# Kernel optimization log

Hardware: AMD Instinct MI355X
Metric: run time of the kernel (lower is better)

## Reference

```python
import jax, jax.numpy as jnp
import numpy as np

B, S, T = 32, 64, 64
D = 512          # model_size == controller hidden == cell_size
R = 4            # read heads
M = 64           # nr_cells
V = 10000        # vocab
IF = R * D + 3 * D + 5 * R + 3   # DNC interface vector size (3607)
NN_IN = D + R * D                # controller input: x + read vectors
CLIP = 20.0
EPS = 1e-6


def _cosine(mem, keys):
    # mem (B,m,w), keys (B,h,w) -> (B,h,m) batched cosine similarity
    mn = mem / (jnp.linalg.norm(mem, axis=2, keepdims=True) + EPS)
    kn = keys / (jnp.linalg.norm(keys, axis=2, keepdims=True) + EPS)
    return jnp.einsum('bhw,bmw->bhm', kn, mn)


def _allocate(usage):
    # usage (B,m) -> allocation weights (B,1,m)
    u = EPS + (1.0 - EPS) * usage
    phi = jnp.argsort(u, axis=1)                      # ascending: least used first
    su = jnp.take_along_axis(u, phi, axis=1)
    excl = jnp.cumprod(jnp.concatenate([jnp.ones_like(su[:, :1]), su[:, :-1]], axis=1), axis=1)
    sa = (1.0 - su) * excl
    return jnp.take_along_axis(sa, jnp.argsort(phi, axis=1), axis=1)[:, None, :]


def _memory_step(xi, st):
    memory, link, prec, rw, ww, usage = st
    b = xi.shape[0]
    # --- parse interface vector (same slicing as dnc.Memory, independent_linears=False) ---
    rk = jnp.tanh(xi[:, :R * D].reshape(b, R, D))                        # read keys
    rs = jax.nn.softplus(xi[:, R * D:R * D + R])                         # read strengths
    wk = jnp.tanh(xi[:, R * D + R:R * D + R + D].reshape(b, 1, D))       # write key
    ws = jax.nn.softplus(xi[:, R * D + R + D])[:, None]                  # write strength
    er = jax.nn.sigmoid(xi[:, R * D + R + D + 1:R * D + R + 2 * D + 1].reshape(b, 1, D))
    wv = jnp.tanh(xi[:, R * D + R + 2 * D + 1:R * D + R + 3 * D + 1].reshape(b, 1, D))
    fg = jax.nn.sigmoid(xi[:, R * D + R + 3 * D + 1:R * D + 2 * R + 3 * D + 1])   # free gates
    ag = jax.nn.sigmoid(xi[:, R * D + 2 * R + 3 * D + 1])[:, None, None]          # alloc gate
    wg = jax.nn.sigmoid(xi[:, R * D + 2 * R + 3 * D + 2])[:, None, None]          # write gate
    modes = jax.nn.softmax(xi[:, R * D + 2 * R + 3 * D + 3:R * D + 5 * R + 3 * D + 3].reshape(b, R, 3), axis=2)
    # --- write ---
    usage = usage + (1 - usage) * (1 - jnp.prod(1 - ww, axis=1))
    usage = usage * jnp.prod(1 - fg[:, :, None] * rw, axis=1)
    wcw = jax.nn.softmax(_cosine(memory, wk) * ws[:, :, None], axis=2)   # (B,1,M)
    alloc = _allocate(usage)
    ww = wg * (ag * alloc + (1 - ag) * wcw)                              # (B,1,M)
    reset = jnp.prod(1 - ww[:, :, :, None] * er[:, :, None, :], axis=1)  # (B,M,D)
    memory = memory * reset + jnp.einsum('bhm,bhw->bmw', ww, wv)
    ww_i, ww_j = ww[:, :, :, None], ww[:, :, None, :]
    link = (1 - ww_i - ww_j) * link + ww_i * prec[:, :, None, :]
    link = link * (1 - jnp.eye(M, dtype=link.dtype))                     # zero diagonal
    prec = (1 - jnp.sum(ww, axis=2, keepdims=True)) * prec + ww
    # --- read ---
    cw = jax.nn.softmax(_cosine(memory, rk) * rs[:, :, None], axis=2)    # (B,R,M)
    l0 = link[:, 0]
    fwd = jnp.einsum('bnm,brm->brn', l0, rw)
    bwd = jnp.einsum('bmn,brm->brn', l0, rw)
    rw = modes[:, :, 0:1] * bwd + modes[:, :, 1:2] * fwd + modes[:, :, 2:3] * cw
    rv = jnp.einsum('brm,bmw->brw', rw, memory)                          # read vectors
    return (memory, link, prec, rw, ww, usage), rv


def _lstm_cell(x, h, c, Wih, Whh, bih, bhh):
    g = x @ Wih.T + bih + h @ Whh.T + bhh
    i, f, gg, o = jnp.split(g, 4, axis=-1)
    c2 = jax.nn.sigmoid(f) * c + jax.nn.sigmoid(i) * jnp.tanh(gg)
    return jax.nn.sigmoid(o) * jnp.tanh(c2), c2


def _dnc_run(x, p, mem0):
    # x: (B,L,D). Faithful to ixaxaar dnc.py: each timestep input is concat(x_t, initial last_read=zeros).
    b, L, _ = x.shape
    xin = jnp.concatenate([x, jnp.zeros((b, L, R * D), x.dtype)], axis=-1)
    h = jnp.zeros((2, b, D), x.dtype)
    c = jnp.zeros((2, b, D), x.dtype)

    def step(carry, x_t):
        (h, c), mem = carry
        h0, c0 = _lstm_cell(x_t, h[0], c[0], p['Wih0'], p['Whh0'], p['bih0'], p['bhh0'])
        h1, c1 = _lstm_cell(h0, h[1], c[1], p['Wih1'], p['Whh1'], p['bih1'], p['bhh1'])
        out = jnp.clip(h1, -CLIP, CLIP)
        xi = out @ p['Wi'].T + p['bi']
        mem, rv = _memory_step(xi, mem)
        full = jnp.concatenate([out, rv.reshape(b, R * D)], axis=-1)
        y = full @ p['Wo'].T + p['bo']
        return ((jnp.stack([h0, h1]), jnp.stack([c0, c1])), mem), y

    (_, memT), ys = jax.lax.scan(step, ((h, c), mem0), jnp.swapaxes(xin, 0, 1))
    return jnp.swapaxes(ys, 0, 1), memT


def _init_mem(b, dtype):
    return (jnp.zeros((b, M, D), dtype), jnp.zeros((b, 1, M, M), dtype),
            jnp.zeros((b, 1, M), dtype), jnp.zeros((b, R, M), dtype),
            jnp.zeros((b, 1, M), dtype), jnp.zeros((b, M), dtype))


_PNAMES = ['Wih0', 'Whh0', 'bih0', 'bhh0', 'Wih1', 'Whh1', 'bih1', 'bhh1', 'Wi', 'bi', 'Wo', 'bo']


def setup_inputs() -> dict:
    key = jax.random.key(0)
    ks = iter(jax.random.split(key, 40))

    def p(shape, s=0.05):
        return jax.random.normal(next(ks), shape, dtype=jnp.float32) * s

    d = {'emb_src': p((V, D), 0.5), 'emb_tgt': p((V, D), 0.5)}
    shapes = [(4 * D, NN_IN), (4 * D, D), (4 * D,), (4 * D,), (4 * D, D), (4 * D, D), (4 * D,), (4 * D,),
              (IF, D), (IF,), (D, NN_IN), (D,)]
    for pre in ('enc', 'dec'):
        for n, sh in zip(_PNAMES, shapes):
            d[pre + '_' + n] = p(sh)
    d['fc_W'] = p((V, D))
    d['fc_b'] = p((V,))
    d['input'] = jax.random.randint(next(ks), (B, S), 0, V, dtype=jnp.int32)
    d['tgt'] = jax.random.randint(next(ks), (B, T), 0, V, dtype=jnp.int32)
    return d


def reference(emb_src, emb_tgt,
              enc_Wih0, enc_Whh0, enc_bih0, enc_bhh0, enc_Wih1, enc_Whh1, enc_bih1, enc_bhh1,
              enc_Wi, enc_bi, enc_Wo, enc_bo,
              dec_Wih0, dec_Whh0, dec_bih0, dec_bhh0, dec_Wih1, dec_Whh1, dec_bih1, dec_bhh1,
              dec_Wi, dec_bi, dec_Wo, dec_bo,
              fc_W, fc_b, input, tgt):
    enc_vals = [enc_Wih0, enc_Whh0, enc_bih0, enc_bhh0, enc_Wih1, enc_Whh1, enc_bih1, enc_bhh1,
                enc_Wi, enc_bi, enc_Wo, enc_bo]
    dec_vals = [dec_Wih0, dec_Whh0, dec_bih0, dec_bhh0, dec_Wih1, dec_Whh1, dec_bih1, dec_bhh1,
                dec_Wi, dec_bi, dec_Wo, dec_bo]
    enc_p = dict(zip(_PNAMES, enc_vals))
    dec_p = dict(zip(_PNAMES, dec_vals))
    src = emb_src[input]                                   # (B,S,D)
    _, mem = _dnc_run(src, enc_p, _init_mem(src.shape[0], src.dtype))
    out, _ = _dnc_run(emb_tgt[tgt], dec_p, mem)            # decoder reuses encoder memory state
    logits = out @ fc_W.T + fc_b                           # (B,T,V)
    return jnp.transpose(logits, (0, 2, 1))                # (B,V,T)
```

## Files before the change

kernel.cpp:

```cpp
#include <hip/hip_runtime.h>

#define BB   32
#define DD   512
#define RR   4
#define MM   64
#define VV   10000
#define TT   64
#define IFX  3607
#define NNIN 2560
#define EPSF 1e-6f

typedef unsigned short u16;

__device__ __forceinline__ float bf(u16 u){ return __uint_as_float(((unsigned)u)<<16); }
__device__ __forceinline__ float4 b4f(ushort4 u){
  float4 f; f.x = bf(u.x); f.y = bf(u.y); f.z = bf(u.z); f.w = bf(u.w); return f;
}
__device__ __forceinline__ u16 f2b(float f){
  unsigned u = __float_as_uint(f);
  u += 0x7fffu + ((u>>16)&1u);
  return (u16)(u>>16);
}
__device__ __forceinline__ float sigmf(float x){ return 1.f/(1.f+__expf(-x)); }
__device__ __forceinline__ float softplusf(float x){ return x > 20.f ? x : log1pf(__expf(x)); }
__device__ __forceinline__ float wredSum(float v){
  #pragma unroll
  for (int s=1;s<64;s<<=1) v += __shfl_xor(v,s,64);
  return v;
}
__device__ __forceinline__ float wredMax(float v){
  #pragma unroll
  for (int s=1;s<64;s<<=1) v = fmaxf(v, __shfl_xor(v,s,64));
  return v;
}

__device__ __forceinline__ float ldg_c(const float* p){
  return __hip_atomic_load(const_cast<float*>(p), __ATOMIC_RELAXED, __HIP_MEMORY_SCOPE_AGENT);
}
__device__ __forceinline__ void stg_c(float* p, float v){
  __hip_atomic_store(p, v, __ATOMIC_RELAXED, __HIP_MEMORY_SCOPE_AGENT);
}
__device__ __forceinline__ unsigned ldg_cu(const unsigned* p){
  return __hip_atomic_load(const_cast<unsigned*>(p), __ATOMIC_RELAXED, __HIP_MEMORY_SCOPE_AGENT);
}
__device__ __forceinline__ void stg_cu(unsigned* p, unsigned v){
  __hip_atomic_store(p, v, __ATOMIC_RELAXED, __HIP_MEMORY_SCOPE_AGENT);
}

__device__ __forceinline__ void ldg_cv4x2(const float* p0,const float* p1, float4& a,float4& b){
  asm volatile("global_load_dwordx4 %0, %2, off sc0 sc1\n\t"
               "global_load_dwordx4 %1, %3, off sc0 sc1\n\t"
               "s_waitcnt vmcnt(0)"
               : "=&v"(a),"=&v"(b)
               : "v"(p0),"v"(p1)
               : "memory");
}
__device__ __forceinline__ void ldg_issue2(const float* p0,const float* p1, float4& a,float4& b){
  asm volatile("global_load_dwordx4 %0, %2, off sc0 sc1\n\t"
               "global_load_dwordx4 %1, %3, off sc0 sc1"
               : "=&v"(a),"=&v"(b)
               : "v"(p0),"v"(p1)
               : "memory");
}
__device__ __forceinline__ void ld_fence(){
  asm volatile("s_waitcnt vmcnt(0)" ::: "memory");
}
__device__ __forceinline__ void ldg_c4s(const float* p0,const float* p1,const float* p2,const float* p3,
                                        float& a,float& b,float& c,float& d){
  asm volatile("global_load_dword %0, %4, off sc0 sc1\n\t"
               "global_load_dword %1, %5, off sc0 sc1\n\t"
               "global_load_dword %2, %6, off sc0 sc1\n\t"
               "global_load_dword %3, %7, off sc0 sc1\n\t"
               "s_waitcnt vmcnt(0)"
               : "=&v"(a),"=&v"(b),"=&v"(c),"=&v"(d)
               : "v"(p0),"v"(p1),"v"(p2),"v"(p3)
               : "memory");
}
__device__ __forceinline__ void ldg_c2s(const float* p0,const float* p1, float& a,float& b){
  asm volatile("global_load_dword %0, %2, off sc0 sc1\n\t"
               "global_load_dword %1, %3, off sc0 sc1\n\t"
               "s_waitcnt vmcnt(0)"
               : "=&v"(a),"=&v"(b)
               : "v"(p0),"v"(p1)
               : "memory");
}

#define SM_FLOATS 9600
#define NBLK 256u
#define NTHR 512

__device__ __forceinline__ void gbar5(unsigned* flags, unsigned* gen, unsigned ep){
  asm volatile("s_waitcnt vmcnt(0) lgkmcnt(0)" ::: "memory");
  __syncthreads();
  if (threadIdx.x == 0) stg_cu(&flags[blockIdx.x*16], ep);
  if (blockIdx.x == 0) {
    if (threadIdx.x < 256) {
      const unsigned* f = &flags[threadIdx.x*16];
      while (ldg_cu(f) < ep) __builtin_amdgcn_s_sleep(1);
    }
    __syncthreads();
    if (threadIdx.x == 0) stg_cu(gen, ep);
  } else if (threadIdx.x == 0) {
    while (ldg_cu(gen) < ep) __builtin_amdgcn_s_sleep(1);
  }
  __syncthreads();
}

#define LW_OFF 5312
#define XW_OFF 4224

__device__ __forceinline__ void preload_lstm(float* S, int tile,
    const float* __restrict__ Wx, int wx_stride, const float* __restrict__ Wh)
{
  float* WL = S + LW_OFF;
  const int tid = threadIdx.x;
  const int dblk = tile*8;
  for (int i = tid; i < 8192; i += NTHR) {
    const int r  = i >> 8;
    const int k4 = (i & 255) * 4;
    const int gr = ((r>>3)<<9) + dblk + (r&7);
    float4 v;
    if (k4 < 512) v = *(const float4*)&Wx[(size_t)gr*wx_stride + k4];
    else          v = *(const float4*)&Wh[(size_t)gr*512 + (k4-512)];
    *(float4*)&WL[r*1028 + k4] = v;
  }
}

__device__ __forceinline__ void preload_xi(float* S, int xtile, const float* __restrict__ Wi){
  float* XW = S + XW_OFF;
  const int tid = threadIdx.x;
  for (int i = tid; i < 8192; i += NTHR) {
    const int r  = i >> 7;
    const int k4 = (i & 127) * 4;
    int cr = xtile*64 + r; if (cr >= IFX) cr = IFX-1;
    *(float4*)&XW[r*516 + k4] = *(const float4*)&Wi[(size_t)cr*512 + k4];
  }
}

__device__ __noinline__ void lstm_tile_p(
    float* S, int tile,
    const float* __restrict__ bx, const float* __restrict__ bh,
    const float* emb, const int* seq, int t,
    const float* xf,
    const float* hprev, float* hcur,
    float* cst, float* outc, u16* full)
{
  float (*As)[132] = (float(*)[132])S;
  float* gs = S + 4224;
  int* idxs = (int*)(S + 5280);
  const float* WL = S + LW_OFF;
  const int tid = threadIdx.x;
  const int c  = tid >> 4;
  const int b2 = tid & 15;
  const int dblk = tile * 8;
  const int gcol = ((c>>3)<<9) + dblk + (c&7);
  const int ba = tid >> 5;
  const int bbs = ba + 16;
  const int f0 = (tid & 31) * 4;
  float a0p=0.f, a0q=0.f, a1p=0.f, a1q=0.f;
  if (emb != nullptr && tid < 32) idxs[tid] = seq[tid*64 + t];
  __syncthreads();
  #define LSRC(ch, bb_) ( ((ch) < 4) \
      ? ((emb != nullptr) ? &emb[(size_t)idxs[bb_]*512 + (ch)*128 + f0] \
                          : &xf[(bb_)*512 + (ch)*128 + f0]) \
      : &hprev[(bb_)*512 + ((ch)*128 - 512) + f0] )
  float4 v0, v1;
  ldg_cv4x2(LSRC(0,ba), LSRC(0,bbs), v0, v1);
  *(float4*)&As[ba][f0]  = v0;
  *(float4*)&As[bbs][f0] = v1;
  __syncthreads();
  for (int chunk = 0; chunk < 8; ++chunk) {
    if (chunk < 7) ldg_issue2(LSRC(chunk+1,ba), LSRC(chunk+1,bbs), v0, v1);
    const float* Wr = WL + c*1028 + chunk*128;
    #pragma unroll 8
    for (int kk = 0; kk < 128; kk += 4) {
      const float4 w4 = *(const float4*)&Wr[kk];
      const float4 x0 = *(const float4*)&As[b2][kk];
      const float4 x1 = *(const float4*)&As[b2+16][kk];
      a0p = fmaf(x0.x,w4.x, fmaf(x0.y,w4.y, a0p));
      a0q = fmaf(x0.z,w4.z, fmaf(x0.w,w4.w, a0q));
      a1p = fmaf(x1.x,w4.x, fmaf(x1.y,w4.y, a1p));
      a1q = fmaf(x1.z,w4.z, fmaf(x1.w,w4.w, a1q));
    }
    __syncthreads();
    if (chunk < 7) {
      ld_fence();
      *(float4*)&As[ba][f0]  = v0;
      *(float4*)&As[bbs][f0] = v1;
    }
    __syncthreads();
  }
  #undef LSRC
  const float bias = bx[gcol] + bh[gcol];
  gs[c*33 + b2]      = a0p + a0q + bias;
  gs[c*33 + b2 + 16] = a1p + a1q + bias;
  __syncthreads();
  if (tid < 256) {
    const int bb2 = tid & 31, dl2 = tid >> 5;
    const float gi = gs[(0*8+dl2)*33 + bb2];
    const float gf = gs[(1*8+dl2)*33 + bb2];
    const float gg = gs[(2*8+dl2)*33 + bb2];
    const float go = gs[(3*8+dl2)*33 + bb2];
    const int d = dblk + dl2;
    const int cid = bb2*512 + d;
    const float cv = sigmf(gf)*cst[cid] + sigmf(gi)*tanhf(gg);
    const float hv = sigmf(go)*tanhf(cv);
    cst[cid] = cv;
    stg_c(&hcur[cid], hv);
    if (outc != nullptr) {
      const float oc = fminf(fmaxf(hv,-20.f),20.f);
      stg_c(&outc[cid], oc);
      if (full != nullptr) full[((size_t)t*32 + bb2)*2560 + d] = f2b(oc);
    }
  }
  __syncthreads();
}

__device__ __noinline__ void xi_tile_p(
    float* S, int xtile,
    const float* outc, const float* __restrict__ bi, float* xi)
{
  float (*As)[132] = (float(*)[132])S;
  const float* XW = S + XW_OFF;
  const int tid = threadIdx.x;
  const int c  = tid >> 3;
  const int bq = tid & 7;
  const int col = xtile*64 + c;
  const int ba = tid >> 5;
  const int bbs = ba + 16;
  const int f0 = (tid & 31) * 4;
  float accp[4], accq[4];
  #pragma unroll
  for (int j=0;j<4;j++){ accp[j]=0.f; accq[j]=0.f; }
  float4 v0, v1;
  ldg_cv4x2(&outc[ba*512 + f0], &outc[bbs*512 + f0], v0, v1);
  *(float4*)&As[ba][f0]  = v0;
  *(float4*)&As[bbs][f0] = v1;
  __syncthreads();
  for (int chunk = 0; chunk < 4; ++chunk) {
    if (chunk < 3) {
      const int kn = (chunk+1)*128;
      ldg_issue2(&outc[ba*512 + kn + f0], &outc[bbs*512 + kn + f0], v0, v1);
    }
    const float* Wr = XW + c*516 + chunk*128;
    #pragma unroll 4
    for (int kk = 0; kk < 128; kk += 4) {
      const float4 w4 = *(const float4*)&Wr[kk];
      #pragma unroll
      for (int m=0;m<4;m++){
        const float4 a = *(const float4*)&As[bq + 8*m][kk];
        accp[m] = fmaf(a.x,w4.x, fmaf(a.y,w4.y, accp[m]));
        accq[m] = fmaf(a.z,w4.z, fmaf(a.w,w4.w, accq[m]));
      }
    }
    __syncthreads();
    if (chunk < 3) {
      ld_fence();
      *(float4*)&As[ba][f0]  = v0;
      *(float4*)&As[bbs][f0] = v1;
    }
    __syncthreads();
  }
  if (col < IFX) {
    const float bias = bi[col];
    #pragma unroll
    for (int m=0;m<4;m++)
      stg_c(&xi[(size_t)(bq + 8*m)*IFX + col], accp[m] + accq[m] + bias);
  }
  __syncthreads();
}

__device__ __constant__ int kSidx[23] = {
  2048,2049,2050,2051, 2564, 3589,3590,3591,3592, 3593, 3594,
  3595,3596,3597, 3598,3599,3600, 3601,3602,3603, 3604,3605,3606
};

#define MEMPITCH 516
#define L_MEM   0
#define L_LINK  33024
#define L_RK    37184
#define L_WK    39232
#define L_RWP   39744
#define L_PREC  40000
#define L_USAGE 40064
#define L_WCW   40128
#define L_U     40192
#define L_WW    40256
#define L_CWA   40320
#define L_SC    40576
#define L_SRAW  40616
#define L_END   40640
#define DYN_LDS_BYTES 162560

__device__ __noinline__ void mem_tile_lds(
    float* S, int b, const float* xi, u16* full, int t)
{
  const int tid = threadIdx.x;
  const float* xb = xi + (size_t)b*IFX;
  float* MEMS = S + L_MEM;
  float* LNK  = S + L_LINK;
  float (*rk_s)[512] = (float(*)[512])(S + L_RK);
  float* wk_s  = S + L_WK;
  float* RWP   = S + L_RWP;
  float* PREC  = S + L_PREC;
  float* USAGE = S + L_USAGE;
  float* wcw_s = S + L_WCW;
  float* u_s   = S + L_U;
  float* WW    = S + L_WW;
  float* sorted_s = S + L_CWA;
  float* excl_s   = S + L_CWA + 64;
  int*   rank_s   = (int*)(S + L_CWA + 128);
  float (*cw_s)[64] = (float(*)[64])(S + L_CWA);
  float* sc   = S + L_SC;
  float* sraw = S + L_SRAW;

  {
    const float* base = xb + tid*4;
    float v0,v1,v2,v3;
    ldg_c4s(base+0,base+1,base+2,base+3, v0,v1,v2,v3);
    float* d = &rk_s[tid>>7][(tid&127)*4];
    d[0]=tanhf(v0); d[1]=tanhf(v1); d[2]=tanhf(v2); d[3]=tanhf(v3);
  }
  if (tid < 128) {
    const float* base = xb + 2052 + tid*4;
    float v0,v1,v2,v3;
    ldg_c4s(base+0,base+1,base+2,base+3, v0,v1,v2,v3);
    float* d = &wk_s[tid*4];
    d[0]=tanhf(v0); d[1]=tanhf(v1); d[2]=tanhf(v2); d[3]=tanhf(v3);
  }
  if (tid < 23) sraw[tid] = ldg_c(&xb[kSidx[tid]]);
  __syncthreads();
  if (tid == 0) {
    for (int r=0;r<4;r++) sc[r] = softplusf(sraw[r]);
    sc[4] = softplusf(sraw[4]);
    for (int r=0;r<4;r++) sc[5+r] = sigmf(sraw[5+r]);
    sc[9]  = sigmf(sraw[9]);
    sc[10] = sigmf(sraw[10]);
    for (int r=0;r<4;r++) {
      const float a0=sraw[11+3*r], a1=sraw[12+3*r], a2=sraw[13+3*r];
      const float mx=fmaxf(a0,fmaxf(a1,a2));
      const float e0=__expf(a0-mx), e1=__expf(a1-mx), e2=__expf(a2-mx);
      const float s=e0+e1+e2;
      sc[11+3*r]=e0/s; sc[12+3*r]=e1/s; sc[13+3*r]=e2/s;
    }
  }
  if (tid < 256) {
    const int wid = tid>>6, ln = tid&63;
    float p = 0.f;
    for (int i = ln; i < 512; i += 64) { const float v = rk_s[wid][i]; p = fmaf(v,v,p); }
    p = wredSum(p);
    if (ln == 0) sc[24+wid] = sqrtf(p);
    if (wid == 1) {
      float q2 = 0.f;
      for (int i = ln; i < 512; i += 64) { const float v = wk_s[i]; q2 = fmaf(v,v,q2); }
      q2 = wredSum(q2);
      if (ln == 0) sc[23] = sqrtf(q2);
    }
  }
  __syncthreads();
  if (tid < 256) {
    const int m = tid>>2, q = tid&3;
    const float* mr = MEMS + m*MEMPITCH;
    float d = 0.f, ss = 0.f;
    for (int i = q*128; i < q*128+128; i += 4) {
      const float4 mv = *(const float4*)&mr[i];
      d = fmaf(mv.x, wk_s[i  ], d); d = fmaf(mv.y, wk_s[i+1], d);
      d = fmaf(mv.z, wk_s[i+2], d); d = fmaf(mv.w, wk_s[i+3], d);
      ss = fmaf(mv.x,mv.x,ss); ss = fmaf(mv.y,mv.y,ss);
      ss = fmaf(mv.z,mv.z,ss); ss = fmaf(mv.w,mv.w,ss);
    }
    d  += __shfl_xor(d,1,64);  d  += __shfl_xor(d,2,64);
    ss += __shfl_xor(ss,1,64); ss += __shfl_xor(ss,2,64);
    if (q == 0) wcw_s[m] = d / ((sqrtf(ss)+EPSF)*(sc[23]+EPSF)) * sc[4];
  }
  if (tid < 64) {
    const float uo = USAGE[tid];
    float u = uo + (1.f-uo)*WW[tid];
    #pragma unroll
    for (int r=0;r<4;r++) u *= (1.f - sc[5+r]*RWP[r*64+tid]);
    USAGE[tid] = u;
  }
  __syncthreads();
  if (tid < 64) {
    const float v = wcw_s[tid];
    const float mx = wredMax(v);
    const float e = __expf(v-mx);
    const float s2 = wredSum(e);
    wcw_s[tid] = e/s2;
    u_s[tid] = EPSF + (1.f-EPSF)*USAGE[tid];
  }
  __syncthreads();
  if (tid < 64) {
    const float u = u_s[tid]; int rk2 = 0;
    for (int j=0;j<64;j++){ const float uj = u_s[j]; rk2 += (uj<u) || (uj==u && j<tid); }
    rank_s[tid] = rk2; sorted_s[rk2] = u;
  }
  __syncthreads();
  if (tid == 0) { float run = 1.f; for (int p2=0;p2<64;p2++){ excl_s[p2]=run; run*=sorted_s[p2]; } }
  __syncthreads();
  if (tid < 64) {
    const float al = (1.f - u_s[tid]) * excl_s[rank_s[tid]];
    const float wwv = sc[10]*(sc[9]*al + (1.f-sc[9])*wcw_s[tid]);
    WW[tid] = wwv;
    const float s3 = wredSum(wwv);
    if (tid==0) sc[28] = s3;
  }
  __syncthreads();
  {
    float e0,w0;
    ldg_c2s(&xb[2565+tid], &xb[3077+tid], e0, w0);
    const float er0 = sigmf(e0);
    const float wv0 = tanhf(w0);
    #pragma unroll 4
    for (int m=0;m<64;m++){
      const float wwm = WW[m];
      float* p = MEMS + m*MEMPITCH + tid;
      p[0] = p[0]*(1.f - wwm*er0) + wwm*wv0;
    }
  }
  __syncthreads();
  for (int e = tid; e < 4096; e += NTHR) {
    const int i2 = e>>6, j2 = e&63;
    const float lv = LNK[i2*65+j2];
    LNK[i2*65+j2] = (i2==j2) ? 0.f
               : ((1.f - WW[i2] - WW[j2])*lv + WW[i2]*PREC[j2]);
  }
  __syncthreads();
  if (tid < 64) PREC[tid] = (1.f - sc[28])*PREC[tid] + WW[tid];
  __syncthreads();
  const int r6 = tid>>6, m6 = tid&63;
  if (tid < 256) {
    const float* mr = MEMS + m6*MEMPITCH;
    const float* rkr = rk_s[r6];
    float d = 0.f, ss = 0.f;
    for (int i=0;i<512;i+=4){
      const float4 mv = *(const float4*)&mr[i];
      d = fmaf(mv.x, rkr[i  ], d); d = fmaf(mv.y, rkr[i+1], d);
      d = fmaf(mv.z, rkr[i+2], d); d = fmaf(mv.w, rkr[i+3], d);
      ss = fmaf(mv.x,mv.x,ss); ss = fmaf(mv.y,mv.y,ss);
      ss = fmaf(mv.z,mv.z,ss); ss = fmaf(mv.w,mv.w,ss);
    }
    const float cv = d / ((sqrtf(ss)+EPSF)*(sc[24+r6]+EPSF)) * sc[r6];
    const float mx = wredMax(cv);
    const float e = __expf(cv-mx);
    const float s2 = wredSum(e);
    cw_s[r6][m6] = e/s2;
  }
  __syncthreads();
  float rn = 0.f;
  if (tid < 256) {
    float fw = 0.f, bw = 0.f;
    #pragma unroll 8
    for (int m3=0;m3<64;m3++){
      const float rp = RWP[r6*64+m3];
      fw = fmaf(LNK[m6*65+m3], rp, fw);
      bw = fmaf(LNK[m3*65+m6], rp, bw);
    }
    rn = sc[11+3*r6]*bw + sc[12+3*r6]*fw + sc[13+3*r6]*cw_s[r6][m6];
  }
  __syncthreads();
  if (tid < 256) RWP[r6*64+m6] = rn;
  __syncthreads();
  if (full != nullptr && tid < 256) {
    const int l = tid&63, r8 = tid>>6;
    float a[8];
    #pragma unroll
    for (int j=0;j<8;j++) a[j]=0.f;
    for (int m3=0;m3<64;m3++){
      const float rv_ = RWP[r8*64+m3];
      const float* mr = MEMS + m3*MEMPITCH + 2*l;
      #pragma unroll
      for (int j=0;j<4;j++){
        const float2 v = *(const float2*)&mr[128*j];
        a[2*j]   = fmaf(rv_, v.x, a[2*j]);
        a[2*j+1] = fmaf(rv_, v.y, a[2*j+1]);
      }
    }
    u16* dst = full + ((size_t)t*32 + b)*2560 + 512 + r8*512;
    #pragma unroll
    for (int j=0;j<4;j++){
      const unsigned wd = (unsigned)f2b(a[2*j]) | ((unsigned)f2b(a[2*j+1])<<16);
      *(unsigned*)&dst[2*l + 128*j] = wd;
    }
  }
  __syncthreads();
}

__device__ __noinline__ void lstm_tile_g(
    float* sm, int tile,
    const float* __restrict__ Wx, int wx_stride,
    const float* __restrict__ Wh,
    const float* __restrict__ bx, const float* __restrict__ bh,
    const float* emb, const int* seq, int t,
    const float* xf,
    const float* hprev, float* hcur,
    float* cst, float* outc, u16* full)
{
  float (*As)[132] = (float(*)[132])sm;
  float (*Ws)[132] = (float(*)[132])(sm + 4224);
  float* gs = sm + 8448;
  int* idxs = (int*)(sm + 9504);
  const int tid = threadIdx.x;
  const int c = tid & 31;
  const int dblk = tile * 8;
  const int gcol = ((c>>3)<<9) + dblk + (c&7);
  const int b0 = (tid >> 5) * 4;
  float acc0=0.f, acc1=0.f, acc2=0.f, acc3=0.f;
  if (emb != nullptr && tid < 32) idxs[tid] = seq[tid*64 + t];
  __syncthreads();
  for (int chunk = 0; chunk < 8; ++chunk) {
    const int k0 = chunk * 128;
    const bool xp = (chunk < 4);
    for (int i = tid; i < 1024; i += 256) {
      const int bb2 = i >> 5, f4i = (i & 31)*4;
      if (xp && emb != nullptr) {
        *(float4*)&As[bb2][f4i] = *(const float4*)&emb[(size_t)idxs[bb2]*512 + k0 + f4i];
      } else {
        const float* src = xp ? &xf[bb2*512 + k0 + f4i]
                              : &hprev[bb2*512 + (k0-512) + f4i];
        As[bb2][f4i+0] = ldg_c(src+0);
        As[bb2][f4i+1] = ldg_c(src+1);
        As[bb2][f4i+2] = ldg_c(src+2);
        As[bb2][f4i+3] = ldg_c(src+3);
      }
    }
    for (int i = tid; i < 1024; i += 256) {
      const int r = i >> 5, f4i = (i & 31)*4;
      const int gr = ((r>>3)<<9) + dblk + (r&7);
      const float4 v = xp ? *(const float4*)&Wx[(size_t)gr*wx_stride + k0 + f4i]
                          : *(const float4*)&Wh[(size_t)gr*512 + (k0-512) + f4i];
      *(float4*)&Ws[r][f4i] = v;
    }
    __syncthreads();
    #pragma unroll 8
    for (int kk = 0; kk < 128; kk += 4) {
      const float4 w4 = *(const float4*)&Ws[c][kk];
      const float4 a0 = *(const float4*)&As[b0+0][kk];
      const float4 a1 = *(const float4*)&As[b0+1][kk];
      const float4 a2 = *(const float4*)&As[b0+2][kk];
      const float4 a3 = *(const float4*)&As[b0+3][kk];
      acc0 = fmaf(a0.x,w4.x,fmaf(a0.y,w4.y,fmaf(a0.z,w4.z,fmaf(a0.w,w4.w,acc0))));
      acc1 = fmaf(a1.x,w4.x,fmaf(a1.y,w4.y,fmaf(a1.z,w4.z,fmaf(a1.w,w4.w,acc1))));
      acc2 = fmaf(a2.x,w4.x,fmaf(a2.y,w4.y,fmaf(a2.z,w4.z,fmaf(a2.w,w4.w,acc2))));
      acc3 = fmaf(a3.x,w4.x,fmaf(a3.y,w4.y,fmaf(a3.z,w4.z,fmaf(a3.w,w4.w,acc3))));
    }
    __syncthreads();
  }
  const float bias = bx[gcol] + bh[gcol];
  gs[c*33 + b0+0] = acc0 + bias;
  gs[c*33 + b0+1] = acc1 + bias;
  gs[c*33 + b0+2] = acc2 + bias;
  gs[c*33 + b0+3] = acc3 + bias;
  __syncthreads();
  {
    const int b2 = tid & 31, dl2 = tid >> 5;
    const float gi = gs[(0*8+dl2)*33 + b2];
    const float gf = gs[(1*8+dl2)*33 + b2];
    const float gg = gs[(2*8+dl2)*33 + b2];
    const float go = gs[(3*8+dl2)*33 + b2];
    const int d = dblk + dl2;
    const int cid = b2*512 + d;
    const float cv = sigmf(gf)*cst[cid] + sigmf(gi)*tanhf(gg);
    const float hv = sigmf(go)*tanhf(cv);
    cst[cid] = cv;
    stg_c(&hcur[cid], hv);
    if (outc != nullptr) {
      const float oc = fminf(fmaxf(hv,-20.f),20.f);
      stg_c(&outc[cid], oc);
      if (full != nullptr) full[((size_t)t*32 + b2)*2560 + d] = f2b(oc);
    }
// ... 555 lines not shown
```

Measured before the change: 4.279 ms.

## Register-tile LSTM and interface GEMM tiles with split-K shuffle reduction

Reworks the per-step LSTM gate and interface-vector matmul tiles so each thread computes a 4x4 register block over a slice of K, then combines partial sums with wave shuffles. This cuts LDS reads per FMA and removes the shared-memory gate staging buffer in the LSTM tile. It also drops the prefetch of the next activation chunk and goes back to a blocking load per chunk, which may expose global-load latency on the serial recurrent path.

```diff
diff --git a/kernel.cpp b/kernel.cpp
--- a/kernel.cpp
+++ b/kernel.cpp
@@ -54,16 +54,6 @@
                : "=&v"(a),"=&v"(b)
                : "v"(p0),"v"(p1)
                : "memory");
-}
-__device__ __forceinline__ void ldg_issue2(const float* p0,const float* p1, float4& a,float4& b){
-  asm volatile("global_load_dwordx4 %0, %2, off sc0 sc1\n\t"
-               "global_load_dwordx4 %1, %3, off sc0 sc1"
-               : "=&v"(a),"=&v"(b)
-               : "v"(p0),"v"(p1)
-               : "memory");
-}
-__device__ __forceinline__ void ld_fence(){
-  asm volatile("s_waitcnt vmcnt(0)" ::: "memory");
 }
 __device__ __forceinline__ void ldg_c4s(const float* p0,const float* p1,const float* p2,const float* p3,
                                         float& a,float& b,float& c,float& d){
@@ -146,71 +136,89 @@
     float* cst, float* outc, u16* full)
 {
   float (*As)[132] = (float(*)[132])S;
-  float* gs = S + 4224;
   int* idxs = (int*)(S + 5280);
   const float* WL = S + LW_OFF;
   const int tid = threadIdx.x;
-  const int c  = tid >> 4;
-  const int b2 = tid & 15;
+  const int w  = tid >> 6;
+  const int bg = (tid >> 3) & 7;
+  const int ks = tid & 7;
   const int dblk = tile * 8;
-  const int gcol = ((c>>3)<<9) + dblk + (c&7);
   const int ba = tid >> 5;
   const int bbs = ba + 16;
   const int f0 = (tid & 31) * 4;
-  float a0p=0.f, a0q=0.f, a1p=0.f, a1q=0.f;
+  float acc[4][4];
+  #pragma unroll
+  for (int i=0;i<4;i++)
+    #pragma unroll
+    for (int j=0;j<4;j++) acc[i][j]=0.f;
   if (emb != nullptr && tid < 32) idxs[tid] = seq[tid*64 + t];
   __syncthreads();
   #define LSRC(ch, bb_) ( ((ch) < 4) \
       ? ((emb != nullptr) ? &emb[(size_t)idxs[bb_]*512 + (ch)*128 + f0] \
                           : &xf[(bb_)*512 + (ch)*128 + f0]) \
       : &hprev[(bb_)*512 + ((ch)*128 - 512) + f0] )
-  float4 v0, v1;
-  ldg_cv4x2(LSRC(0,ba), LSRC(0,bbs), v0, v1);
-  *(float4*)&As[ba][f0]  = v0;
-  *(float4*)&As[bbs][f0] = v1;
-  __syncthreads();
   for (int chunk = 0; chunk < 8; ++chunk) {
-    if (chunk < 7) ldg_issue2(LSRC(chunk+1,ba), LSRC(chunk+1,bbs), v0, v1);
-    const float* Wr = WL + c*1028 + chunk*128;
-    #pragma unroll 8
-    for (int kk = 0; kk < 128; kk += 4) {
-      const float4 w4 = *(const float4*)&Wr[kk];
-      const float4 x0 = *(const float4*)&As[b2][kk];
-      const float4 x1 = *(const float4*)&As[b2+16][kk];
-      a0p = fmaf(x0.x,w4.x, fmaf(x0.y,w4.y, a0p));
-      a0q = fmaf(x0.z,w4.z, fmaf(x0.w,w4.w, a0q));
-      a1p = fmaf(x1.x,w4.x, fmaf(x1.y,w4.y, a1p));
-      a1q = fmaf(x1.z,w4.z, fmaf(x1.w,w4.w, a1q));
-    }
-    __syncthreads();
-    if (chunk < 7) {
-      ld_fence();
+    {
+      float4 v0, v1;
+      ldg_cv4x2(LSRC(chunk,ba), LSRC(chunk,bbs), v0, v1);
       *(float4*)&As[ba][f0]  = v0;
       *(float4*)&As[bbs][f0] = v1;
     }
     __syncthreads();
+    const int kb = chunk*128;
+    #pragma unroll
+    for (int m = 0; m < 4; ++m) {
+      const int kk = ks*4 + m*32;
+      float4 w4[4], a4[4];
+      #pragma unroll
+      for (int j=0;j<4;j++) w4[j] = *(const float4*)&WL[(w + 8*j)*1028 + kb + kk];
+      #pragma unroll
+      for (int i=0;i<4;i++) a4[i] = *(const float4*)&As[bg + 8*i][kk];
+      #pragma unroll
+      for (int i=0;i<4;i++)
+        #pragma unroll
+        for (int j=0;j<4;j++)
+          acc[i][j] = fmaf(a4[i].x,w4[j].x, fmaf(a4[i].y,w4[j].y,
+                      fmaf(a4[i].z,w4[j].z, fmaf(a4[i].w,w4[j].w, acc[i][j]))));
+    }
+    __syncthreads();
   }
   #undef LSRC
-  const float bias = bx[gcol] + bh[gcol];
-  gs[c*33 + b2]      = a0p + a0q + bias;
-  gs[c*33 + b2 + 16] = a1p + a1q + bias;
-  __syncthreads();
-  if (tid < 256) {
-    const int bb2 = tid & 31, dl2 = tid >> 5;
-    const float gi = gs[(0*8+dl2)*33 + bb2];
-    const float gf = gs[(1*8+dl2)*33 + bb2];
-    const float gg = gs[(2*8+dl2)*33 + bb2];
-    const float go = gs[(3*8+dl2)*33 + bb2];
-    const int d = dblk + dl2;
-    const int cid = bb2*512 + d;
-    const float cv = sigmf(gf)*cst[cid] + sigmf(gi)*tanhf(gg);
-    const float hv = sigmf(go)*tanhf(cv);
-    cst[cid] = cv;
-    stg_c(&hcur[cid], hv);
-    if (outc != nullptr) {
-      const float oc = fminf(fmaxf(hv,-20.f),20.f);
-      stg_c(&outc[cid], oc);
-      if (full != nullptr) full[((size_t)t*32 + bb2)*2560 + d] = f2b(oc);
+  #pragma unroll
+  for (int i=0;i<4;i++)
+    #pragma unroll
+    for (int j=0;j<4;j++){
+      float v = acc[i][j];
+      v += __shfl_xor(v,1,64);
+      v += __shfl_xor(v,2,64);
+      v += __shfl_xor(v,4,64);
+      acc[i][j] = v;
+    }
+  if (ks == 0) {
+    const int d = dblk + w;
+    float bias[4];
+    #pragma unroll
+    for (int j=0;j<4;j++){
+      const int gcol = (j<<9) + d;
+      bias[j] = bx[gcol] + bh[gcol];
+    }
+    #pragma unroll
+    for (int i=0;i<4;i++){
+      const int b = bg + 8*i;
+      const int cid = b*512 + d;
+      const float gi = acc[i][0] + bias[0];
+      const float gf = acc[i][1] + bias[1];
+      const float gg = acc[i][2] + bias[2];
+      const float go = acc[i][3] + bias[3];
+      const float cv = sigmf(gf)*cst[cid] + sigmf(gi)*tanhf(gg);
+      const float hv = sigmf(go)*tanhf(cv);
+      cst[cid] = cv;
+      stg_c(&hcur[cid], hv);
+      if (outc != nullptr) {
+        const float oc = fminf(fmaxf(hv,-20.f),20.f);
+        stg_c(&outc[cid], oc);
+        if (full != nullptr) full[((size_t)t*32 + b)*2560 + d] = f2b(oc);
+      }
     }
   }
   __syncthreads();
@@ -223,49 +231,67 @@
   float (*As)[132] = (float(*)[132])S;
   const float* XW = S + XW_OFF;
   const int tid = threadIdx.x;
-  const int c  = tid >> 3;
-  const int bq = tid & 7;
-  const int col = xtile*64 + c;
+  const int w  = tid >> 6;
+  const int l  = tid & 63;
+  const int tt = l >> 2;
+  const int ks = l & 3;
+  const int cg = 2*w + (tt>>3);
+  const int bg = tt & 7;
   const int ba = tid >> 5;
   const int bbs = ba + 16;
   const int f0 = (tid & 31) * 4;
-  float accp[4], accq[4];
+  float acc[4][4];
   #pragma unroll
-  for (int j=0;j<4;j++){ accp[j]=0.f; accq[j]=0.f; }
-  float4 v0, v1;
-  ldg_cv4x2(&outc[ba*512 + f0], &outc[bbs*512 + f0], v0, v1);
-  *(float4*)&As[ba][f0]  = v0;
-  *(float4*)&As[bbs][f0] = v1;
-  __syncthreads();
+  for (int i=0;i<4;i++)
+    #pragma unroll
+    for (int j=0;j<4;j++) acc[i][j]=0.f;
   for (int chunk = 0; chunk < 4; ++chunk) {
-    if (chunk < 3) {
-      const int kn = (chunk+1)*128;
-      ldg_issue2(&outc[ba*512 + kn + f0], &outc[bbs*512 + kn + f0], v0, v1);
-    }
-    const float* Wr = XW + c*516 + chunk*128;
-    #pragma unroll 4
-    for (int kk = 0; kk < 128; kk += 4) {
-      const float4 w4 = *(const float4*)&Wr[kk];
-      #pragma unroll
-      for (int m=0;m<4;m++){
-        const float4 a = *(const float4*)&As[bq + 8*m][kk];
-        accp[m] = fmaf(a.x,w4.x, fmaf(a.y,w4.y, accp[m]));
-        accq[m] = fmaf(a.z,w4.z, fmaf(a.w,w4.w, accq[m]));
-      }
-    }
-    __syncthreads();
-    if (chunk < 3) {
-      ld_fence();
+    {
+      const int kb0 = chunk*128;
+      float4 v0, v1;
+      ldg_cv4x2(&outc[ba*512 + kb0 + f0], &outc[bbs*512 + kb0 + f0], v0, v1);
       *(float4*)&As[ba][f0]  = v0;
       *(float4*)&As[bbs][f0] = v1;
     }
     __syncthreads();
-  }
-  if (col < IFX) {
-    const float bias = bi[col];
-    #pragma unroll
-    for (int m=0;m<4;m++)
-      stg_c(&xi[(size_t)(bq + 8*m)*IFX + col], accp[m] + accq[m] + bias);
+    const int kb = chunk*128;
+    #pragma unroll
+    for (int m = 0; m < 8; ++m) {
+      const int kk = ks*4 + m*16;
+      float4 w4[4], a4[4];
+      #pragma unroll
+      for (int j=0;j<4;j++) w4[j] = *(const float4*)&XW[(cg + 16*j)*516 + kb + kk];
+      #pragma unroll
+      for (int i=0;i<4;i++) a4[i] = *(const float4*)&As[bg + 8*i][kk];
+      #pragma unroll
+      for (int i=0;i<4;i++)
+        #pragma unroll
+        for (int j=0;j<4;j++)
+          acc[i][j] = fmaf(a4[i].x,w4[j].x, fmaf(a4[i].y,w4[j].y,
+                      fmaf(a4[i].z,w4[j].z, fmaf(a4[i].w,w4[j].w, acc[i][j]))));
+    }
+    __syncthreads();
+  }
+  #pragma unroll
+  for (int i=0;i<4;i++)
+    #pragma unroll
+    for (int j=0;j<4;j++){
+      float v = acc[i][j];
+      v += __shfl_xor(v,1,64);
+      v += __shfl_xor(v,2,64);
+      acc[i][j] = v;
+    }
+  if (ks == 0) {
+    #pragma unroll
+    for (int j=0;j<4;j++){
+      const int col = xtile*64 + cg + 16*j;
+      if (col < IFX) {
+        const float bias = bi[col];
+        #pragma unroll
+        for (int i=0;i<4;i++)
+          stg_c(&xi[(size_t)(bg + 8*i)*IFX + col], acc[i][j] + bias);
+      }
+    }
   }
   __syncthreads();
 }
```

New measurement: 4.249 ms. About the same (-0.7%).
